# Performance work log

Measured on AMD Instinct MI355X. Metric: run time of the kernel, lower is better.

## Reference

```python
import jax, jax.numpy as jnp
import numpy as np

N_COMPONENTS = 3  # sklearn PCA(n_components=3); X is [C=3, T] so n_samples = 3


def _pca_bvp(X):
    """Replicates sklearn PCA.fit on X [C, T]; returns components_[1] * explained_variance_[1]."""
    C = X.shape[0]
    Xc = X - X.mean(axis=0, keepdims=True)          # center features (column means)
    U, S, Vt = jnp.linalg.svd(Xc, full_matrices=False)  # U [C,C], S [C], Vt [C,T]
    # sklearn svd_flip: sign of the max-|.|
    # element of each column of U fixes the sign of the corresponding row of Vt
    idx = jnp.argmax(jnp.abs(U), axis=0)             # [C]
    signs = jnp.sign(U[idx, jnp.arange(U.shape[1])])
    signs = jnp.where(signs == 0, 1.0, signs)
    Vt = Vt * signs[:, None]
    explained_variance = (S * S) / (C - 1)           # [C]
    return Vt[1] * explained_variance[1]             # [T]


def setup_inputs() -> dict:
    key = jax.random.key(0)
    x = jax.random.normal(key, (8, 3, 512, 64, 64), dtype=jnp.float32)
    return {"x": x}


def reference(x):
    # x: [B, C, T, H, W] -> spatial mean -> [B, C, T]
    xm = jnp.mean(x, axis=(3, 4))
    # batched per-sample PCA (fuses the original per-sample CPU sklearn loop)
    return jax.vmap(_pca_bvp)(xm)  # [B, T]
```

## Files before the change

kernel.cpp:

```cpp
#include <hip/hip_runtime.h>
#include <math.h>

typedef float fvec4 __attribute__((ext_vector_type(4)));

__global__ __launch_bounds__(512) void mean_kernel(const float* __restrict__ x,
                                                   float* __restrict__ m) {
    const int wave = threadIdx.x >> 6;
    const int lane = threadIdx.x & 63;
    const int row  = blockIdx.x * 8 + wave;
    const fvec4* p = (const fvec4*)(x + (size_t)row * 4096);

    fvec4 v[16];
#pragma unroll
    for (int k = 0; k < 16; ++k)
        v[k] = __builtin_nontemporal_load(&p[lane + 64 * k]);

    float s = 0.f;
#pragma unroll
    for (int k = 0; k < 16; ++k)
        s += (v[k].x + v[k].y) + (v[k].z + v[k].w);

    for (int off = 32; off; off >>= 1) s += __shfl_down(s, off, 64);

    if (lane == 0) m[row] = s * (1.0f / 4096.0f);
}

__global__ __launch_bounds__(512) void pca_kernel(const float* __restrict__ m,
                                                  float* __restrict__ out) {
    const int b = blockIdx.x;
    const int t = threadIdx.x;
    const float* X = m + b * 3 * 512;

    const float x0 = X[t], x1 = X[512 + t], x2 = X[1024 + t];
    const float mu = (x0 + x1 + x2) * (1.0f / 3.0f);
    const float c0 = x0 - mu, c1 = x1 - mu, c2 = x2 - mu;

    float g[6] = { c0 * c0, c0 * c1, c0 * c2, c1 * c1, c1 * c2, c2 * c2 };

    __shared__ float red[8][6];
#pragma unroll
    for (int j = 0; j < 6; ++j) {
        float v = g[j];
        for (int off = 32; off; off >>= 1) v += __shfl_down(v, off, 64);
        g[j] = v;
    }
    const int wave = t >> 6, lane = t & 63;
    if (lane == 0) {
#pragma unroll
        for (int j = 0; j < 6; ++j) red[wave][j] = g[j];
    }
    __syncthreads();

    __shared__ float coef[3];
    if (t == 0) {
        double G[6] = {0, 0, 0, 0, 0, 0};
        for (int w = 0; w < 8; ++w)
            for (int j = 0; j < 6; ++j) G[j] += (double)red[w][j];
        const double a00 = G[0], a01 = G[1], a02 = G[2];
        const double a11 = G[3], a12 = G[4], a22 = G[5];

        const double q = (a00 + a11 + a22) / 3.0;
        const double b00 = a00 - q, b11 = a11 - q, b22 = a22 - q;
        const double p2 = b00 * b00 + b11 * b11 + b22 * b22
                        + 2.0 * (a01 * a01 + a02 * a02 + a12 * a12);
        double p = sqrt(p2 / 6.0);
        double l1;
        if (p < 1e-300) {
            l1 = q;
        } else {
            const double pinv = 1.0 / p;
            const double d00 = b00 * pinv, d11 = b11 * pinv, d22 = b22 * pinv;
            const double d01 = a01 * pinv, d02 = a02 * pinv, d12 = a12 * pinv;
            double r = 0.5 * (d00 * (d11 * d22 - d12 * d12)
                            - d01 * (d01 * d22 - d12 * d02)
                            + d02 * (d01 * d12 - d11 * d02));
            r = fmin(1.0, fmax(-1.0, r));
            const double phi = acos(r) / 3.0;
            const double l_max = q + 2.0 * p * cos(phi);
            const double l_min = q + 2.0 * p * cos(phi + 2.0943951023931953);
            l1 = 3.0 * q - l_max - l_min;
        }

        const double r0x = a00 - l1, r0y = a01,      r0z = a02;
        const double r1x = a01,      r1y = a11 - l1, r1z = a12;
        const double r2x = a02,      r2y = a12,      r2z = a22 - l1;

        double vax = r0y * r1z - r0z * r1y;
        double vay = r0z * r1x - r0x * r1z;
        double vaz = r0x * r1y - r0y * r1x;
        double vbx = r0y * r2z - r0z * r2y;
        double vby = r0z * r2x - r0x * r2z;
        double vbz = r0x * r2y - r0y * r2x;
        double vcx = r1y * r2z - r1z * r2y;
        double vcy = r1z * r2x - r1x * r2z;
        double vcz = r1x * r2y - r1y * r2x;

        const double na = vax * vax + vay * vay + vaz * vaz;
        const double nb = vbx * vbx + vby * vby + vbz * vbz;
        const double nc = vcx * vcx + vcy * vcy + vcz * vcz;

        double vx = vax, vy = vay, vz = vaz, n = na;
        if (nb > n) { vx = vbx; vy = vby; vz = vbz; n = nb; }
        if (nc > n) { vx = vcx; vy = vcy; vz = vcz; n = nc; }
        const double ninv = (n > 0.0) ? (1.0 / sqrt(n)) : 0.0;
        vx *= ninv; vy *= ninv; vz *= ninv;

        int idx = 0;
        double best = fabs(vx);
        if (fabs(vy) > best) { best = fabs(vy); idx = 1; }
        if (fabs(vz) > best) { best = fabs(vz); idx = 2; }
        const double comp = (idx == 0) ? vx : (idx == 1) ? vy : vz;
        const double s = (comp >= 0.0) ? 1.0 : -1.0;

        const double scale = s * 0.5 * sqrt(fmax(l1, 0.0));
        coef[0] = (float)(vx * scale);
        coef[1] = (float)(vy * scale);
        coef[2] = (float)(vz * scale);
    }
    __syncthreads();

    out[b * 512 + t] = coef[0] * c0 + coef[1] * c1 + coef[2] * c2;
}

extern "C" void kernel_launch(void* const* d_in, const int* in_sizes, int n_in,
                              void* d_out, int out_size, void* d_ws, size_t ws_size,
                              hipStream_t stream) {
    const float* x = (const float*)d_in[0];
    float* out = (float*)d_out;
    float* m = (float*)d_ws;

    const int ROWS = 8 * 3 * 512;
    mean_kernel<<<ROWS / 8, 512, 0, stream>>>(x, m);
    pca_kernel<<<8, 512, 0, stream>>>(m, out);
}
```

Before: 254.1 us.

## Fuse mean and PCA kernels using last-block atomic counter

Merges the spatial-mean kernel and the per-sample PCA kernel into a single launch. Each block increments a global counter after writing its means, and the last block to finish performs the PCA for all 8 samples, one wave per sample. This removes a kernel launch and the gap between the two kernels, but adds a memset, an atomic plus fences in every block, and a serialized PCA tail run by a single block.

```diff
diff --git a/kernel.cpp b/kernel.cpp
--- a/kernel.cpp
+++ b/kernel.cpp
@@ -3,8 +3,10 @@
 
 typedef float fvec4 __attribute__((ext_vector_type(4)));
 
-__global__ __launch_bounds__(512) void mean_kernel(const float* __restrict__ x,
-                                                   float* __restrict__ m) {
+__global__ __launch_bounds__(512) void fused_kernel(const float* __restrict__ x,
+                                                    float* __restrict__ m,
+                                                    unsigned int* __restrict__ counter,
+                                                    float* __restrict__ out) {
     const int wave = threadIdx.x >> 6;
     const int lane = threadIdx.x & 63;
     const int row  = blockIdx.x * 8 + wave;
@@ -21,43 +23,47 @@
         s += (v[k].x + v[k].y) + (v[k].z + v[k].w);
 
     for (int off = 32; off; off >>= 1) s += __shfl_down(s, off, 64);
+    if (lane == 0) m[row] = s * (1.0f / 4096.0f);
 
-    if (lane == 0) m[row] = s * (1.0f / 4096.0f);
-}
-
-__global__ __launch_bounds__(512) void pca_kernel(const float* __restrict__ m,
-                                                  float* __restrict__ out) {
-    const int b = blockIdx.x;
-    const int t = threadIdx.x;
-    const float* X = m + b * 3 * 512;
-
-    const float x0 = X[t], x1 = X[512 + t], x2 = X[1024 + t];
-    const float mu = (x0 + x1 + x2) * (1.0f / 3.0f);
-    const float c0 = x0 - mu, c1 = x1 - mu, c2 = x2 - mu;
-
-    float g[6] = { c0 * c0, c0 * c1, c0 * c2, c1 * c1, c1 * c2, c2 * c2 };
-
-    __shared__ float red[8][6];
-#pragma unroll
-    for (int j = 0; j < 6; ++j) {
-        float v = g[j];
-        for (int off = 32; off; off >>= 1) v += __shfl_down(v, off, 64);
-        g[j] = v;
-    }
-    const int wave = t >> 6, lane = t & 63;
-    if (lane == 0) {
-#pragma unroll
-        for (int j = 0; j < 6; ++j) red[wave][j] = g[j];
+    __shared__ int sh_last;
+    __syncthreads();
+    if (threadIdx.x == 0) {
+        __threadfence();
+        unsigned old = atomicAdd(counter, 1u);
+        sh_last = (old == (unsigned)(gridDim.x - 1));
     }
     __syncthreads();
+    if (!sh_last) return;
+    __threadfence();
 
-    __shared__ float coef[3];
-    if (t == 0) {
-        double G[6] = {0, 0, 0, 0, 0, 0};
-        for (int w = 0; w < 8; ++w)
-            for (int j = 0; j < 6; ++j) G[j] += (double)red[w][j];
-        const double a00 = G[0], a01 = G[1], a02 = G[2];
-        const double a11 = G[3], a12 = G[4], a22 = G[5];
+    const int b = wave;
+    const float* X = m + b * 1536;
+
+    float c0v[8], c1v[8], c2v[8];
+    float g0 = 0, g1 = 0, g2 = 0, g3 = 0, g4 = 0, g5 = 0;
+#pragma unroll
+    for (int k = 0; k < 8; ++k) {
+        const int col = lane + 64 * k;
+        const float x0 = X[col], x1 = X[512 + col], x2 = X[1024 + col];
+        const float mu = (x0 + x1 + x2) * (1.0f / 3.0f);
+        const float c0 = x0 - mu, c1 = x1 - mu, c2 = x2 - mu;
+        c0v[k] = c0; c1v[k] = c1; c2v[k] = c2;
+        g0 += c0 * c0; g1 += c0 * c1; g2 += c0 * c2;
+        g3 += c1 * c1; g4 += c1 * c2; g5 += c2 * c2;
+    }
+    for (int off = 32; off; off >>= 1) {
+        g0 += __shfl_down(g0, off, 64);
+        g1 += __shfl_down(g1, off, 64);
+        g2 += __shfl_down(g2, off, 64);
+        g3 += __shfl_down(g3, off, 64);
+        g4 += __shfl_down(g4, off, 64);
+        g5 += __shfl_down(g5, off, 64);
+    }
+
+    float cf0 = 0.f, cf1 = 0.f, cf2 = 0.f;
+    if (lane == 0) {
+        const double a00 = g0, a01 = g1, a02 = g2;
+        const double a11 = g3, a12 = g4, a22 = g5;
 
         const double q = (a00 + a11 + a22) / 3.0;
         const double b00 = a00 - q, b11 = a11 - q, b22 = a22 - q;
@@ -110,16 +116,20 @@
         if (fabs(vy) > best) { best = fabs(vy); idx = 1; }
         if (fabs(vz) > best) { best = fabs(vz); idx = 2; }
         const double comp = (idx == 0) ? vx : (idx == 1) ? vy : vz;
-        const double s = (comp >= 0.0) ? 1.0 : -1.0;
+        const double sg = (comp >= 0.0) ? 1.0 : -1.0;
 
-        const double scale = s * 0.5 * sqrt(fmax(l1, 0.0));
-        coef[0] = (float)(vx * scale);
-        coef[1] = (float)(vy * scale);
-        coef[2] = (float)(vz * scale);
+        const double scale = sg * 0.5 * sqrt(fmax(l1, 0.0));
+        cf0 = (float)(vx * scale);
+        cf1 = (float)(vy * scale);
+        cf2 = (float)(vz * scale);
     }
-    __syncthreads();
+    cf0 = __shfl(cf0, 0, 64);
+    cf1 = __shfl(cf1, 0, 64);
+    cf2 = __shfl(cf2, 0, 64);
 
-    out[b * 512 + t] = coef[0] * c0 + coef[1] * c1 + coef[2] * c2;
+#pragma unroll
+    for (int k = 0; k < 8; ++k)
+        out[b * 512 + lane + 64 * k] = cf0 * c0v[k] + cf1 * c1v[k] + cf2 * c2v[k];
 }
 
 extern "C" void kernel_launch(void* const* d_in, const int* in_sizes, int n_in,
@@ -127,9 +137,12 @@
                               hipStream_t stream) {
     const float* x = (const float*)d_in[0];
     float* out = (float*)d_out;
-    float* m = (float*)d_ws;
+
+    unsigned int* counter = (unsigned int*)d_ws;
+    float* m = (float*)((char*)d_ws + 1024);
+
+    hipMemsetAsync(d_ws, 0, 4, stream);
 
     const int ROWS = 8 * 3 * 512;
-    mean_kernel<<<ROWS / 8, 512, 0, stream>>>(x, m);
-    pca_kernel<<<8, 512, 0, stream>>>(m, out);
+    fused_kernel<<<ROWS / 8, 512, 0, stream>>>(x, m, counter, out);
 }
```

Result: slower. 333.0 us (+31.0%).
